# Kernel optimization log

Hardware: AMD Instinct MI355X
Metric: run time of the kernel (lower is better)

Reference implementation:

```python
import jax, jax.numpy as jnp
import numpy as np

B, N, D = 8, 2048, 1024
DC = 1024          # d_center
K = 4              # num_centers
NUM_JUMPS = 2
SPAN = 2
FIN = (2 + 2 * NUM_JUMPS + 1) * D  # 7*D

def _gelu(x):
    return jax.nn.gelu(x, approximate=False)  # torch nn.GELU default is exact erf

def setup_inputs() -> dict:
    key = jax.random.key(0)
    ks = jax.random.split(key, 16)
    s = lambda k, *sh: jax.random.normal(k, sh, dtype=jnp.float32) * 0.02
    return {
        "queries": jax.random.normal(ks[0], (B, N, D), dtype=jnp.float32),
        "fr_w1": s(ks[1], FIN, D), "fr_b1": jnp.zeros((D,), jnp.float32),
        "fr_w2": s(ks[2], D, D),   "fr_b2": jnp.zeros((D,), jnp.float32),
        "tc_w1": s(ks[3], D, DC),  "tc_b1": jnp.zeros((DC,), jnp.float32),
        "tc_w2": s(ks[4], DC, DC), "tc_b2": jnp.zeros((DC,), jnp.float32),
        "centers": jax.random.normal(ks[5], (K, DC), dtype=jnp.float32),
        "fc_w1": s(ks[6], D + DC, D), "fc_b1": jnp.zeros((D,), jnp.float32),
        "fc_w2": s(ks[7], D, D),      "fc_b2": jnp.zeros((D,), jnp.float32),
        "g_w": s(ks[8], D + DC, D),   "g_b": jnp.zeros((D,), jnp.float32),
    }

def reference(queries, fr_w1, fr_b1, fr_w2, fr_b2,
              tc_w1, tc_b1, tc_w2, tc_b2, centers,
              fc_w1, fc_b1, fc_w2, fc_b2, g_w, g_b):
    x = queries
    shifts = [1, -1, 0]  # left, right, x
    for i in range(1, NUM_JUMPS + 1):
        shifts += [i * SPAN, -i * SPAN]
    fusion = jnp.concatenate([jnp.roll(x, s, axis=1) for s in shifts], axis=-1)  # [B,N,7D]
    x_ring = _gelu(fusion @ fr_w1 + fr_b1) @ fr_w2 + fr_b2                       # [B,N,D]
    token_proj = _gelu(x_ring @ tc_w1 + tc_b1) @ tc_w2 + tc_b2                   # [B,N,DC]
    w = jax.nn.softmax(jnp.einsum('bnd,kd->bnk', token_proj, centers), axis=-1)  # [B,N,K]
    weighted = jnp.einsum('bnk,kd->bnd', w, centers)                             # [B,N,DC]
    fus2 = jnp.concatenate([x_ring, weighted], axis=-1)                          # [B,N,D+DC]
    gate = jax.nn.sigmoid(fus2 @ g_w + g_b)
    fc = _gelu(fus2 @ fc_w1 + fc_b1) @ fc_w2 + fc_b2
    return gate * fc + (1.0 - gate) * x_ring
```

## Files before the change

kernel.cpp:

```cpp
#include <hip/hip_runtime.h>
#include <hip/hip_bf16.h>
#include <math.h>

typedef unsigned short u16;
typedef __attribute__((ext_vector_type(8))) short short8;
typedef __attribute__((ext_vector_type(4))) float f32x4;


__device__ __forceinline__ float bf2f(u16 b) {
  return __uint_as_float(((unsigned int)b) << 16);
}
__device__ __forceinline__ u16 f2bf(float f) {
  unsigned int u = __float_as_uint(f);
  u += 0x7FFFu + ((u >> 16) & 1u);
  return (u16)(u >> 16);
}
__device__ __forceinline__ float gelu_exact(float x) {
  return 0.5f * x * (1.0f + erff(x * 0.70710678118654752f));
}

__device__ __forceinline__ void cp16(const void* g, void* l) {
  __builtin_amdgcn_global_load_lds(
      (const __attribute__((address_space(1))) unsigned int*)g,
      (__attribute__((address_space(3))) unsigned int*)l, 16, 0, 0);
}

template <int MODE, bool GATHER>
__global__ __launch_bounds__(512) void gemm256(
    const u16* __restrict__ A, int lda, const u16* __restrict__ Wt, int K,
    const float* __restrict__ bias, const float* __restrict__ bias2,
    void* __restrict__ out0, int ldo0, void* __restrict__ out1,
    void* __restrict__ out2, const float* __restrict__ p0,
    const float* __restrict__ p1, const float* __restrict__ p2) {
  extern __shared__ __align__(16) char sm[];
  const int tid = threadIdx.x;
  const int lane = tid & 63;
  const int wave = tid >> 6;
  const int wm = wave >> 2;
  const int wn = wave & 3;

  const unsigned linear = blockIdx.y * gridDim.x + blockIdx.x;
  const unsigned xcd = linear & 7u;
  const unsigned pos = linear >> 3;
  const unsigned bx = pos % gridDim.x;
  const unsigned by = xcd * (gridDim.y >> 3) + pos / gridDim.x;
  const int m0 = by * 256;
  const int n0 = bx * 256;

  const int sl = lane >> 3;
  const int qqs = (lane & 7) ^ sl;
  const int rowoff = sl * 2 + (qqs >> 2);
  const int colq = qqs & 3;

  const int r16 = lane & 15, q4 = lane >> 4;
  const int qqr = (((r16 & 1) << 2) | q4) ^ (r16 >> 1);
  const int laneA = wm * 8192 + (r16 >> 1) * 128 + qqr * 16;
  const int laneB = wn * 4096 + (r16 >> 1) * 128 + qqr * 16;

  const int nt = K >> 5;

  f32x4 acc[8][4];
#pragma unroll
  for (int i = 0; i < 8; i++)
#pragma unroll
    for (int j = 0; j < 4; j++) acc[i][j] = (f32x4){0.f, 0.f, 0.f, 0.f};

  auto a_src = [&](int t, int i) -> const u16* {
    const int chunk = wave + i * 8;
    const int row = chunk * 16 + rowoff;
    if (GATHER) {
      const int kg = t * 32 + colq * 8;
      const int seg = kg >> 10;
      int shift;
      switch (seg) {
        case 0: shift = 1; break;
        case 1: shift = -1; break;
        case 2: shift = 0; break;
        case 3: shift = 2; break;
        case 4: shift = -2; break;
        case 5: shift = 4; break;
        default: shift = -4; break;
      }
      const int m = m0 + row;
      const int b = m >> 11;
      const int nsrc = ((m & 2047) - shift) & 2047;
      return A + (long)((b << 11) | nsrc) * 1024 + (kg & 1023);
    }
    return A + (long)(m0 + row) * lda + t * 32 + colq * 8;
  };
  auto b_src = [&](int t, int i) -> const u16* {
    const int chunk = wave + i * 8;
    const int row = chunk * 16 + rowoff;
    return Wt + (long)(n0 + row) * K + t * 32 + colq * 8;
  };

  auto prefetch = [&](int s, short8 (&pbf)[4], short8 (&paf01)[2]) {
    const char* base = sm + ((s & 3) << 15);
#pragma unroll
    for (int ni = 0; ni < 4; ni++)
      pbf[ni] = *(const short8*)(base + 16384 + laneB + ni * 1024);
#pragma unroll
    for (int mi = 0; mi < 2; mi++)
      paf01[mi] = *(const short8*)(base + laneA + mi * 1024);
  };

  const u16 *pA0, *pA1, *pB0, *pB1;

  auto body = [&](int s, short8 (&cbf)[4], short8 (&caf01)[2],
                  short8 (&nbf)[4], short8 (&naf01)[2]) {
    const char* abase = sm + ((s & 3) << 15);
    short8 afr[6];
#pragma unroll
    for (int j = 0; j < 6; j++)
      afr[j] = *(const short8*)(abase + laneA + (j + 2) * 1024);
    prefetch(s + 1, nbf, naf01);

    const int sofs = ((s + 3) & 3) << 15;
    cp16(pA0, sm + sofs + wave * 1024);
    cp16(pA1, sm + sofs + (wave + 8) * 1024);
    cp16(pB0, sm + sofs + 16384 + wave * 1024);
    cp16(pB1, sm + sofs + 16384 + (wave + 8) * 1024);
    if (s + 4 <= nt - 1) {
      if (GATHER && (((s + 4) & 31) == 0)) {
        pA0 = a_src(s + 4, 0);
        pA1 = a_src(s + 4, 1);
      } else {
        pA0 += 32;
        pA1 += 32;
      }
      pB0 += 32;
      pB1 += 32;
    }

    asm volatile("s_waitcnt lgkmcnt(12)" ::: "memory");
    __builtin_amdgcn_sched_barrier(0);
    __builtin_amdgcn_s_setprio(1);
#pragma unroll
    for (int mi = 0; mi < 2; mi++)
#pragma unroll
      for (int ni = 0; ni < 4; ni++)
        acc[mi][ni] = __builtin_amdgcn_mfma_f32_16x16x32_bf16(
            caf01[mi], cbf[ni], acc[mi][ni], 0, 0, 0);

    asm volatile("s_waitcnt lgkmcnt(10)" ::: "memory");
    __builtin_amdgcn_sched_barrier(0);
#pragma unroll
    for (int j = 0; j < 2; j++)
#pragma unroll
      for (int ni = 0; ni < 4; ni++)
        acc[2 + j][ni] = __builtin_amdgcn_mfma_f32_16x16x32_bf16(
            afr[j], cbf[ni], acc[2 + j][ni], 0, 0, 0);

    asm volatile("s_waitcnt lgkmcnt(8)" ::: "memory");
    __builtin_amdgcn_sched_barrier(0);
#pragma unroll
    for (int j = 0; j < 2; j++)
#pragma unroll
      for (int ni = 0; ni < 4; ni++)
        acc[4 + j][ni] = __builtin_amdgcn_mfma_f32_16x16x32_bf16(
            afr[2 + j], cbf[ni], acc[4 + j][ni], 0, 0, 0);

    asm volatile("s_waitcnt lgkmcnt(6)" ::: "memory");
    __builtin_amdgcn_sched_barrier(0);
#pragma unroll
    for (int j = 0; j < 2; j++)
#pragma unroll
      for (int ni = 0; ni < 4; ni++)
        acc[6 + j][ni] = __builtin_amdgcn_mfma_f32_16x16x32_bf16(
            afr[4 + j], cbf[ni], acc[6 + j][ni], 0, 0, 0);
    __builtin_amdgcn_s_setprio(0);

    asm volatile("s_waitcnt vmcnt(4)" ::: "memory");
    __builtin_amdgcn_s_barrier();
  };

#pragma unroll
  for (int t = 0; t < 3; t++) {
    cp16(a_src(t, 0), sm + t * 32768 + wave * 1024);
    cp16(a_src(t, 1), sm + t * 32768 + (wave + 8) * 1024);
    cp16(b_src(t, 0), sm + t * 32768 + 16384 + wave * 1024);
    cp16(b_src(t, 1), sm + t * 32768 + 16384 + (wave + 8) * 1024);
  }
  pA0 = a_src(3, 0); pA1 = a_src(3, 1);
  pB0 = b_src(3, 0); pB1 = b_src(3, 1);
  asm volatile("s_waitcnt vmcnt(4)" ::: "memory");
  __builtin_amdgcn_s_barrier();

  short8 bfA[4], afA[2], bfB[4], afB[2];
  prefetch(0, bfA, afA);

  for (int s = 0; s < nt; s += 2) {
    body(s, bfA, afA, bfB, afB);
    body(s + 1, bfB, afB, bfA, afA);
  }
  asm volatile("s_waitcnt vmcnt(0) lgkmcnt(0)" ::: "memory");

  const int ccol = lane & 15;
  const int crow = (lane >> 4) * 4;
#pragma unroll
  for (int mi = 0; mi < 8; mi++) {
#pragma unroll
    for (int r = 0; r < 4; r++) {
      const int m = m0 + wm * 128 + mi * 16 + crow + r;
      float4 wrow;
      if (MODE == 8) wrow = *(const float4*)(p0 + (size_t)m * 4);
#pragma unroll
      for (int ni = 0; ni < 4; ni++) {
        const int n = n0 + wn * 64 + ni * 16 + ccol;
        const float v = acc[mi][ni][r];
        if (MODE == 0) {
          ((u16*)out0)[(long)m * ldo0 + n] = f2bf(gelu_exact(v + bias[n]));
        } else if (MODE == 4) {
          const float g = p0[(long)m * 1024 + n];
          const float xr = p1[(long)m * 1024 + n];
          ((float*)out0)[(long)m * ldo0 + n] =
              g * (v + bias[n]) + (1.0f - g) * xr;
        } else if (MODE == 6) {
          ((u16*)out0)[(long)m * ldo0 + n] = f2bf(v);
        } else if (MODE == 7) {
          if (n < 1024) {
            const float s = v + bias[n];
            ((float*)out1)[(long)m * 1024 + n] = s;
            ((u16*)out0)[(long)m * 1024 + n] = f2bf(s);
          } else {
            const int nn = n - 1024;
            ((u16*)out2)[(long)m * 1024 + nn] = f2bf(gelu_exact(v + bias2[nn]));
          }
        } else if (MODE == 8) {
          if (n < 1024) {
            const float4 g2 = *(const float4*)(p1 + (size_t)n * 4);
            const float s = v + bias[n] + wrow.x * g2.x + wrow.y * g2.y +
                            wrow.z * g2.z + wrow.w * g2.w;
            ((float*)out0)[(long)m * 1024 + n] = 1.0f / (1.0f + expf(-s));
          } else {
            const int nn = n - 1024;
            const float4 f2 = *(const float4*)(p2 + (size_t)nn * 4);
            const float s = v + bias2[nn] + wrow.x * f2.x + wrow.y * f2.y +
                            wrow.z * f2.z + wrow.w * f2.w;
            ((u16*)out1)[(long)m * 1024 + nn] = f2bf(gelu_exact(s));
          }
        }
      }
    }
  }
}

template <int MODE, bool GATHER>
__global__ __launch_bounds__(256) void gemm128(
    const u16* __restrict__ A, int lda, const u16* __restrict__ Wt, int K,
    const float* __restrict__ bias, const float* __restrict__ bias2,
    void* __restrict__ out0, int ldo0, void* __restrict__ out1,
    void* __restrict__ out2, const float* __restrict__ p0,
    const float* __restrict__ p1, const float* __restrict__ p2) {
  __shared__ __align__(16) u16 As[128 * 64];
  __shared__ __align__(16) u16 Bs[128 * 64];

  const int tid = threadIdx.x;
  const int lane = tid & 63;
  const int wave = tid >> 6;
  const int wm = wave >> 1;
  const int wn = wave & 1;

  const unsigned linear = blockIdx.y * gridDim.x + blockIdx.x;
  const unsigned xcd = linear & 7u;
  const unsigned pos = linear >> 3;
  const unsigned bx = pos % gridDim.x;
  const unsigned by = xcd * (gridDim.y >> 3) + pos / gridDim.x;
  const int m0 = by * 128;
  const int n0 = bx * 128;

  const int srow = lane >> 3;
  const int sq = lane & 7;
  const int sqs = sq ^ srow;

  f32x4 acc[4][4];
#pragma unroll
  for (int i = 0; i < 4; i++)
#pragma unroll
    for (int j = 0; j < 4; j++) acc[i][j] = (f32x4){0.f, 0.f, 0.f, 0.f};

  for (int k0 = 0; k0 < K; k0 += 64) {
#pragma unroll
    for (int i = 0; i < 4; i++) {
      const int rloc = wave * 32 + i * 8 + srow;
      const long gofs = (long)(m0 + rloc) * lda + k0 + sqs * 8;
      cp16(A + gofs, &As[(wave * 32 + i * 8) * 64]);
    }
#pragma unroll
    for (int i = 0; i < 4; i++) {
      const int rloc = wave * 32 + i * 8 + srow;
      const long gofs = (long)(n0 + rloc) * K + k0 + sqs * 8;
      cp16(Wt + gofs, &Bs[(wave * 32 + i * 8) * 64]);
    }
    __syncthreads();

    const int q4 = lane >> 4;
    const int r16 = lane & 15;
#pragma unroll
    for (int kk = 0; kk < 2; kk++) {
      short8 af[4], bf[4];
#pragma unroll
      for (int mi = 0; mi < 4; mi++) {
        const int row = wm * 64 + mi * 16 + r16;
        const int q = (kk * 4 + q4) ^ (row & 7);
        af[mi] = *(const short8*)&As[row * 64 + q * 8];
      }
#pragma unroll
      for (int ni = 0; ni < 4; ni++) {
        const int row = wn * 64 + ni * 16 + r16;
        const int q = (kk * 4 + q4) ^ (row & 7);
        bf[ni] = *(const short8*)&Bs[row * 64 + q * 8];
      }
#pragma unroll
      for (int mi = 0; mi < 4; mi++)
#pragma unroll
        for (int ni = 0; ni < 4; ni++)
          acc[mi][ni] = __builtin_amdgcn_mfma_f32_16x16x32_bf16(
              af[mi], bf[ni], acc[mi][ni], 0, 0, 0);
    }
    __syncthreads();
  }

  const int ccol = lane & 15;
  const int crow = (lane >> 4) * 4;
#pragma unroll
  for (int mi = 0; mi < 4; mi++) {
#pragma unroll
    for (int r = 0; r < 4; r++) {
      const int m = m0 + wm * 64 + mi * 16 + crow + r;
#pragma unroll
      for (int ni = 0; ni < 4; ni++) {
        const int n = n0 + wn * 64 + ni * 16 + ccol;
        const float v = acc[mi][ni][r];
        if (MODE == 6) {
          ((u16*)out0)[(long)m * ldo0 + n] = f2bf(v);
        }
      }
    }
  }
}

__global__ __launch_bounds__(256) void cast_bf16(const float* __restrict__ in,
                                                 u16* __restrict__ out, int n4) {
  const long i = (long)blockIdx.x * 256 + threadIdx.x;
  if (i < n4) {
    const float4 v = ((const float4*)in)[i];
    ushort4 o;
    o.x = f2bf(v.x); o.y = f2bf(v.y); o.z = f2bf(v.z); o.w = f2bf(v.w);
    ((ushort4*)out)[i] = o;
  }
}

__global__ __launch_bounds__(256) void transp_bf16(const float* __restrict__ in,
                                                   u16* __restrict__ out, int K,
                                                   int N) {
  __shared__ float tile[32][33];
  const int tx = threadIdx.x & 31;
  const int ty = threadIdx.x >> 5;
  const long r0 = (long)blockIdx.y * 32;
  const long c0 = (long)blockIdx.x * 32;
#pragma unroll
  for (int r = 0; r < 4; r++)
    tile[ty + r * 8][tx] = in[(r0 + ty + r * 8) * N + c0 + tx];
  __syncthreads();
#pragma unroll
  for (int r = 0; r < 4; r++)
    out[(c0 + ty + r * 8) * K + r0 + tx] = f2bf(tile[tx][ty + r * 8]);
}

__global__ __launch_bounds__(256) void transp7(
    const float* __restrict__ s0, const float* __restrict__ s1,
    const float* __restrict__ s2, const float* __restrict__ s3,
    const float* __restrict__ s4, const float* __restrict__ s5,
    const float* __restrict__ s6, u16* __restrict__ d0, u16* __restrict__ d1,
    u16* __restrict__ d2, u16* __restrict__ d3, u16* __restrict__ d4,
    u16* __restrict__ d5, u16* __restrict__ d6) {
  __shared__ float tile[32][33];
  const float* in;
  u16* out;
  switch (blockIdx.z) {
    case 0: in = s0; out = d0; break;
    case 1: in = s1; out = d1; break;
    case 2: in = s2; out = d2; break;
    case 3: in = s3; out = d3; break;
    case 4: in = s4; out = d4; break;
    case 5: in = s5; out = d5; break;
    default: in = s6; out = d6; break;
  }
  const int tx = threadIdx.x & 31;
  const int ty = threadIdx.x >> 5;
  const long r0 = (long)blockIdx.y * 32;
  const long c0 = (long)blockIdx.x * 32;
#pragma unroll
  for (int r = 0; r < 4; r++)
    tile[ty + r * 8][tx] = in[(r0 + ty + r * 8) * 1024 + c0 + tx];
  __syncthreads();
#pragma unroll
  for (int r = 0; r < 4; r++)
    out[(c0 + ty + r * 8) * 1024 + r0 + tx] = f2bf(tile[tx][ty + r * 8]);
}

__global__ __launch_bounds__(256) void fold_all(
    const u16* __restrict__ GbT, const u16* __restrict__ FbT,
    const u16* __restrict__ Wt3, const float* __restrict__ centers,
    const float* __restrict__ fr_b2, const float* __restrict__ tc_b1,
    const float* __restrict__ tc_w2, const float* __restrict__ tc_b2,
    float* __restrict__ G2T, float* __restrict__ F2T, float* __restrict__ c2,
    float* __restrict__ S, float* __restrict__ bc) {
  const int b = blockIdx.x;
  const int wave = threadIdx.x >> 6, lane = threadIdx.x & 63;
  if (b < 256) {
    const int n = b * 4 + wave;
    float g[4] = {0.f, 0.f, 0.f, 0.f}, f[4] = {0.f, 0.f, 0.f, 0.f};
#pragma unroll
    for (int p = 0; p < 2; p++) {
      const int base = p * 512 + lane * 8;
      const short8 gv = *(const short8*)(GbT + (long)n * 1024 + base);
      const short8 fv = *(const short8*)(FbT + (long)n * 1024 + base);
#pragma unroll
      for (int e = 0; e < 8; e++) {
        const float ge = bf2f((u16)gv[e]), fe = bf2f((u16)fv[e]);
#pragma unroll
        for (int k = 0; k < 4; k++) {
          const float c = centers[k * 1024 + base + e];
          g[k] += ge * c;
          f[k] += fe * c;
        }
      }
    }
#pragma unroll
    for (int k = 0; k < 4; k++)
#pragma unroll
      for (int off = 32; off > 0; off >>= 1) {
        g[k] += __shfl_xor(g[k], off);
        f[k] += __shfl_xor(f[k], off);
      }
    if (lane == 0) {
#pragma unroll
      for (int k = 0; k < 4; k++) {
        G2T[n * 4 + k] = g[k];
        F2T[n * 4 + k] = f[k];
      }
    }
  } else if (b < 512) {
    const int j = (b - 256) * 4 + wave;
    float s = 0.f;
#pragma unroll
    for (int p = 0; p < 2; p++) {
      const int base = p * 512 + lane * 8;
      const short8 wv = *(const short8*)(Wt3 + (long)j * 1024 + base);
#pragma unroll
      for (int e = 0; e < 8; e++) s += fr_b2[base + e] * bf2f((u16)wv[e]);
    }
#pragma unroll
    for (int off = 32; off > 0; off >>= 1) s += __shfl_xor(s, off);
    if (lane == 0) c2[j] = s + tc_b1[j];
  } else if (b < 768) {
    const int d = (b - 512) * 4 + wave;
    const float* row = tc_w2 + (long)d * 1024;
    float s0 = 0.f, s1 = 0.f, s2 = 0.f, s3 = 0.f;
    for (int e = lane; e < 1024; e += 64) {
      const float w = row[e];
      s0 += w * centers[e];
      s1 += w * centers[1024 + e];
      s2 += w * centers[2048 + e];
      s3 += w * centers[3072 + e];
    }
#pragma unroll
    for (int off = 32; off > 0; off >>= 1) {
      s0 += __shfl_xor(s0, off);
      s1 += __shfl_xor(s1, off);
      s2 += __shfl_xor(s2, off);
      s3 += __shfl_xor(s3, off);
    }
    if (lane == 0) {
      S[d] = s0; S[1024 + d] = s1; S[2048 + d] = s2; S[3072 + d] = s3;
    }
  } else {
    const int k = wave;
    float s = 0.f;
    for (int e = lane; e < 1024; e += 64) s += tc_b2[e] * centers[k * 1024 + e];
#pragma unroll
    for (int off = 32; off > 0; off >>= 1) s += __shfl_xor(s, off);
    if (lane == 0) bc[k] = s;
  }
}

__global__ __launch_bounds__(256) void centers_kernel(
    const u16* __restrict__ h2, const float* __restrict__ S,
    const float* __restrict__ bc, float* __restrict__ wtok) {
  const int lane = threadIdx.x & 63;
  const int wave = threadIdx.x >> 6;
  const long t = (long)blockIdx.x * 4 + wave;
  const u16* row = h2 + t * 1024;
  float d0 = 0.f, d1 = 0.f, d2 = 0.f, d3 = 0.f;
#pragma unroll
  for (int j = 0; j < 2; j++) {
    const int dbase = j * 512 + lane * 8;
    const short8 v = *(const short8*)(row + dbase);
#pragma unroll
    for (int e = 0; e < 8; e++) {
      const float x = bf2f((u16)v[e]);
      const int d = dbase + e;
      d0 += x * S[d];
      d1 += x * S[1024 + d];
      d2 += x * S[2048 + d];
      d3 += x * S[3072 + d];
    }
  }
#pragma unroll
  for (int off = 32; off > 0; off >>= 1) {
    d0 += __shfl_xor(d0, off);
    d1 += __shfl_xor(d1, off);
    d2 += __shfl_xor(d2, off);
    d3 += __shfl_xor(d3, off);
  }
  if (lane == 0) {
    d0 += bc[0]; d1 += bc[1]; d2 += bc[2]; d3 += bc[3];
    const float mx = fmaxf(fmaxf(d0, d1), fmaxf(d2, d3));
    float e0 = expf(d0 - mx), e1 = expf(d1 - mx), e2 = expf(d2 - mx),
          e3 = expf(d3 - mx);
    const float inv = 1.0f / (e0 + e1 + e2 + e3);
    *(float4*)(wtok + t * 4) = (float4){e0 * inv, e1 * inv, e2 * inv, e3 * inv};
  }
}

extern "C" void kernel_launch(void* const* d_in, const int* in_sizes, int n_in,
                              void* d_out, int out_size, void* d_ws,
                              size_t ws_size, hipStream_t stream) {
  const float* queries = (const float*)d_in[0];
  const float* fr_w1 = (const float*)d_in[1];
  const float* fr_b1 = (const float*)d_in[2];
  const float* fr_w2 = (const float*)d_in[3];
  const float* fr_b2 = (const float*)d_in[4];
  const float* tc_w1 = (const float*)d_in[5];
  const float* tc_b1 = (const float*)d_in[6];
  const float* tc_w2 = (const float*)d_in[7];
  const float* tc_b2 = (const float*)d_in[8];
  const float* centers = (const float*)d_in[9];
  const float* fc_w1 = (const float*)d_in[10];
  const float* fc_b1 = (const float*)d_in[11];
  const float* fc_w2 = (const float*)d_in[12];
  const float* fc_b2 = (const float*)d_in[13];
  const float* g_w = (const float*)d_in[14];
  const float* g_b = (const float*)d_in[15];

  char* ws = (char*)d_ws;
  u16* Wt1 = (u16*)ws; ws += (size_t)7168 * 1024 * 2;
  u16* Wt3 = (u16*)ws; ws += (size_t)1024 * 1024 * 2;
  u16* Wt6 = (u16*)ws; ws += (size_t)1024 * 1024 * 2;
  u16* WtJ = (u16*)ws; ws += (size_t)2048 * 1024 * 2;
  u16* WtG2 = (u16*)ws; ws += (size_t)2048 * 1024 * 2;
  u16* Fw2b = (u16*)ws; ws += (size_t)1024 * 1024 * 2;
  u16* GbT = (u16*)ws; ws += (size_t)1024 * 1024 * 2;
  u16* FbT = (u16*)ws; ws += (size_t)1024 * 1024 * 2;
  u16* Xb = (u16*)ws;  ws += (size_t)16384 * 1024 * 2;
  u16* h1 = (u16*)ws;  ws += (size_t)16384 * 1024 * 2;
  u16* xrb = (u16*)ws; ws += (size_t)16384 * 1024 * 2;
  float* xring = (float*)ws; ws += (size_t)16384 * 1024 * 4;
  float* wtok = (float*)ws; ws += (size_t)16384 * 4 * 4;
  float* S = (float*)ws; ws += (size_t)4 * 1024 * 4;
  float* G2T = (float*)ws; ws += (size_t)1024 * 4 * 4;
  float* F2T = (float*)ws; ws += (size_t)1024 * 4 * 4;
  float* c2 = (float*)ws; ws += (size_t)1024 * 4;
  float* bc = (float*)ws; ws += 16;
  float* gate = (float*)d_out;
  float* out = (float*)d_out;

  static bool attr_set = false;
  if (!attr_set) {
    attr_set = true;
    (void)hipFuncSetAttribute((const void*)gemm256<0, true>,
                              hipFuncAttributeMaxDynamicSharedMemorySize,
                              131072);
    (void)hipFuncSetAttribute((const void*)gemm256<7, false>,
                              hipFuncAttributeMaxDynamicSharedMemorySize,
                              131072);
    (void)hipFuncSetAttribute((const void*)gemm256<8, false>,
                              hipFuncAttributeMaxDynamicSharedMemorySize,
                              131072);
    (void)hipFuncSetAttribute((const void*)gemm256<4, false>,
                              hipFuncAttributeMaxDynamicSharedMemorySize,
                              131072);
  }

  cast_bf16<<<16384, 256, 0, stream>>>(queries, Xb, 16384 * 1024 / 4);
  cast_bf16<<<1024, 256, 0, stream>>>(fr_w2, Fw2b, 1024 * 1024 / 4);
  transp_bf16<<<dim3(32, 224), 256, 0, stream>>>(fr_w1, Wt1, 7168, 1024);
  transp7<<<dim3(32, 32, 7), 256, 0, stream>>>(
      tc_w1, fc_w2, fr_w2, g_w, fc_w1, g_w + (size_t)1024 * 1024,
      fc_w1 + (size_t)1024 * 1024, Wt3, Wt6, WtJ, WtG2,
      WtG2 + (size_t)1024 * 1024, GbT, FbT);
  fold_all<<<769, 256, 0, stream>>>(GbT, FbT, Wt3, centers, fr_b2, tc_b1,
                                    tc_w2, tc_b2, G2T, F2T, c2, S, bc);
  gemm128<6, false><<<dim3(8, 8), 256, 0, stream>>>(
      Wt3, 1024, Fw2b, 1024, nullptr, nullptr, WtJ + (size_t)1024 * 1024, 1024,
      nullptr, nullptr, nullptr, nullptr, nullptr);

  gemm256<0, true><<<dim3(4, 64), 512, 131072, stream>>>(
      Xb, 0, Wt1, 7168, fr_b1, nullptr, h1, 1024, nullptr, nullptr, nullptr,
      nullptr, nullptr);
  gemm256<7, false><<<dim3(8, 64), 512, 131072, stream>>>(
      h1, 1024, WtJ, 1024, fr_b2, c2, xrb, 1024, xring, Xb, nullptr, nullptr,
      nullptr);
  centers_kernel<<<4096, 256, 0, stream>>>(Xb, S, bc, wtok);
  gemm256<8, false><<<dim3(8, 64), 512, 131072, stream>>>(
      xrb, 1024, WtG2, 1024, g_b, fc_b1, gate, 1024, h1, nullptr, wtok, G2T,
      F2T);
  gemm256<4, false><<<dim3(4, 64), 512, 131072, stream>>>(
      h1, 1024, Wt6, 1024, fc_b2, nullptr, out, 1024, nullptr, nullptr, gate,
      xring, nullptr);
}
```

Measured before the change: 770.0 us.

## Switch 256x256 GEMM to 4 waves with 128x128 per-wave tiles

Rebuilds the main bf16 GEMM to run 256 threads (4 waves in a 2x2 grid) instead of 512, so each wave computes a 128x128 output tile (8x8 MFMA fragments) instead of 128x64. This halves B-fragment LDS reads per MFMA and doubles per-thread global-to-LDS copies. The MFMA groups are reordered so the first group issues before the prefetch and copy instructions, with the wait counts adjusted to match. The cost is far higher accumulator register pressure (256 floats per thread) and fewer waves to hide latency, which risks spills or stalls.

Measured after the change: 1.208 ms. 56.9% more time.

```diff
diff --git a/kernel.cpp b/kernel.cpp
--- a/kernel.cpp
+++ b/kernel.cpp
@@ -26,7 +26,7 @@
 }
 
 template <int MODE, bool GATHER>
-__global__ __launch_bounds__(512) void gemm256(
+__global__ __launch_bounds__(256, 1) void gemm256(
     const u16* __restrict__ A, int lda, const u16* __restrict__ Wt, int K,
     const float* __restrict__ bias, const float* __restrict__ bias2,
     void* __restrict__ out0, int ldo0, void* __restrict__ out1,
@@ -36,8 +36,8 @@
   const int tid = threadIdx.x;
   const int lane = tid & 63;
   const int wave = tid >> 6;
-  const int wm = wave >> 2;
-  const int wn = wave & 3;
+  const int wm = wave >> 1;
+  const int wn = wave & 1;
 
   const unsigned linear = blockIdx.y * gridDim.x + blockIdx.x;
   const unsigned xcd = linear & 7u;
@@ -54,19 +54,20 @@
 
   const int r16 = lane & 15, q4 = lane >> 4;
   const int qqr = (((r16 & 1) << 2) | q4) ^ (r16 >> 1);
-  const int laneA = wm * 8192 + (r16 >> 1) * 128 + qqr * 16;
-  const int laneB = wn * 4096 + (r16 >> 1) * 128 + qqr * 16;
+  const int laneRC = (r16 >> 1) * 128 + qqr * 16;
+  const int laneA = wm * 8192 + laneRC;
+  const int laneB = 16384 + wn * 8192 + laneRC;
 
   const int nt = K >> 5;
 
-  f32x4 acc[8][4];
+  f32x4 acc[8][8];
 #pragma unroll
   for (int i = 0; i < 8; i++)
 #pragma unroll
-    for (int j = 0; j < 4; j++) acc[i][j] = (f32x4){0.f, 0.f, 0.f, 0.f};
+    for (int j = 0; j < 8; j++) acc[i][j] = (f32x4){0.f, 0.f, 0.f, 0.f};
 
   auto a_src = [&](int t, int i) -> const u16* {
-    const int chunk = wave + i * 8;
+    const int chunk = wave + i * 4;
     const int row = chunk * 16 + rowoff;
     if (GATHER) {
       const int kg = t * 32 + colq * 8;
@@ -89,104 +90,116 @@
     return A + (long)(m0 + row) * lda + t * 32 + colq * 8;
   };
   auto b_src = [&](int t, int i) -> const u16* {
-    const int chunk = wave + i * 8;
+    const int chunk = wave + i * 4;
     const int row = chunk * 16 + rowoff;
     return Wt + (long)(n0 + row) * K + t * 32 + colq * 8;
   };
 
-  auto prefetch = [&](int s, short8 (&pbf)[4], short8 (&paf01)[2]) {
+  auto prefetch = [&](int s, short8 (&pbf)[8], short8 (&paf)[2]) {
     const char* base = sm + ((s & 3) << 15);
 #pragma unroll
-    for (int ni = 0; ni < 4; ni++)
-      pbf[ni] = *(const short8*)(base + 16384 + laneB + ni * 1024);
+    for (int ni = 0; ni < 8; ni++)
+      pbf[ni] = *(const short8*)(base + laneB + ni * 1024);
 #pragma unroll
     for (int mi = 0; mi < 2; mi++)
-      paf01[mi] = *(const short8*)(base + laneA + mi * 1024);
+      paf[mi] = *(const short8*)(base + laneA + mi * 1024);
   };
 
-  const u16 *pA0, *pA1, *pB0, *pB1;
-
-  auto body = [&](int s, short8 (&cbf)[4], short8 (&caf01)[2],
-                  short8 (&nbf)[4], short8 (&naf01)[2]) {
+  const u16 *pA0, *pA1, *pA2, *pA3, *pB0, *pB1, *pB2, *pB3;
+
+  auto body = [&](int s, short8 (&cbf)[8], short8 (&caf)[2],
+                  short8 (&nbf)[8], short8 (&naf)[2]) {
     const char* abase = sm + ((s & 3) << 15);
     short8 afr[6];
 #pragma unroll
     for (int j = 0; j < 6; j++)
       afr[j] = *(const short8*)(abase + laneA + (j + 2) * 1024);
-    prefetch(s + 1, nbf, naf01);
-
+
+    asm volatile("s_waitcnt lgkmcnt(6)" ::: "memory");
+    __builtin_amdgcn_sched_barrier(0);
+    __builtin_amdgcn_s_setprio(1);
+#pragma unroll
+    for (int mi = 0; mi < 2; mi++)
+#pragma unroll
+      for (int ni = 0; ni < 8; ni++)
+        acc[mi][ni] = __builtin_amdgcn_mfma_f32_16x16x32_bf16(
+            caf[mi], cbf[ni], acc[mi][ni], 0, 0, 0);
+    __builtin_amdgcn_s_setprio(0);
+    __builtin_amdgcn_sched_barrier(0);
+
+    prefetch(s + 1, nbf, naf);
     const int sofs = ((s + 3) & 3) << 15;
-    cp16(pA0, sm + sofs + wave * 1024);
-    cp16(pA1, sm + sofs + (wave + 8) * 1024);
-    cp16(pB0, sm + sofs + 16384 + wave * 1024);
-    cp16(pB1, sm + sofs + 16384 + (wave + 8) * 1024);
+    cp16(pA0, sm + sofs + (wave + 0) * 1024);
+    cp16(pA1, sm + sofs + (wave + 4) * 1024);
+    cp16(pA2, sm + sofs + (wave + 8) * 1024);
+    cp16(pA3, sm + sofs + (wave + 12) * 1024);
+    cp16(pB0, sm + sofs + 16384 + (wave + 0) * 1024);
+    cp16(pB1, sm + sofs + 16384 + (wave + 4) * 1024);
+    cp16(pB2, sm + sofs + 16384 + (wave + 8) * 1024);
+    cp16(pB3, sm + sofs + 16384 + (wave + 12) * 1024);
     if (s + 4 <= nt - 1) {
       if (GATHER && (((s + 4) & 31) == 0)) {
         pA0 = a_src(s + 4, 0);
         pA1 = a_src(s + 4, 1);
+        pA2 = a_src(s + 4, 2);
+        pA3 = a_src(s + 4, 3);
       } else {
-        pA0 += 32;
-        pA1 += 32;
-      }
-      pB0 += 32;
-      pB1 += 32;
-    }
+        pA0 += 32; pA1 += 32; pA2 += 32; pA3 += 32;
+      }
+      pB0 += 32; pB1 += 32; pB2 += 32; pB3 += 32;
+    }
+
+    asm volatile("s_waitcnt lgkmcnt(14)" ::: "memory");
+    __builtin_amdgcn_sched_barrier(0);
+    __builtin_amdgcn_s_setprio(1);
+#pragma unroll
+    for (int j = 0; j < 2; j++)
+#pragma unroll
+      for (int ni = 0; ni < 8; ni++)
+        acc[2 + j][ni] = __builtin_amdgcn_mfma_f32_16x16x32_bf16(
+            afr[j], cbf[ni], acc[2 + j][ni], 0, 0, 0);
+    __builtin_amdgcn_s_setprio(0);
 
     asm volatile("s_waitcnt lgkmcnt(12)" ::: "memory");
     __builtin_amdgcn_sched_barrier(0);
     __builtin_amdgcn_s_setprio(1);
 #pragma unroll
-    for (int mi = 0; mi < 2; mi++)
-#pragma unroll
-      for (int ni = 0; ni < 4; ni++)
-        acc[mi][ni] = __builtin_amdgcn_mfma_f32_16x16x32_bf16(
-            caf01[mi], cbf[ni], acc[mi][ni], 0, 0, 0);
+    for (int j = 0; j < 2; j++)
+#pragma unroll
+      for (int ni = 0; ni < 8; ni++)
+        acc[4 + j][ni] = __builtin_amdgcn_mfma_f32_16x16x32_bf16(
+            afr[2 + j], cbf[ni], acc[4 + j][ni], 0, 0, 0);
+    __builtin_amdgcn_s_setprio(0);
 
     asm volatile("s_waitcnt lgkmcnt(10)" ::: "memory");
     __builtin_amdgcn_sched_barrier(0);
+    __builtin_amdgcn_s_setprio(1);
 #pragma unroll
     for (int j = 0; j < 2; j++)
 #pragma unroll
-      for (int ni = 0; ni < 4; ni++)
-        acc[2 + j][ni] = __builtin_amdgcn_mfma_f32_16x16x32_bf16(
-            afr[j], cbf[ni], acc[2 + j][ni], 0, 0, 0);
-
-    asm volatile("s_waitcnt lgkmcnt(8)" ::: "memory");
-    __builtin_amdgcn_sched_barrier(0);
-#pragma unroll
-    for (int j = 0; j < 2; j++)
-#pragma unroll
-      for (int ni = 0; ni < 4; ni++)
-        acc[4 + j][ni] = __builtin_amdgcn_mfma_f32_16x16x32_bf16(
-            afr[2 + j], cbf[ni], acc[4 + j][ni], 0, 0, 0);
-
-    asm volatile("s_waitcnt lgkmcnt(6)" ::: "memory");
-    __builtin_amdgcn_sched_barrier(0);
-#pragma unroll
-    for (int j = 0; j < 2; j++)
-#pragma unroll
-      for (int ni = 0; ni < 4; ni++)
+      for (int ni = 0; ni < 8; ni++)
         acc[6 + j][ni] = __builtin_amdgcn_mfma_f32_16x16x32_bf16(
             afr[4 + j], cbf[ni], acc[6 + j][ni], 0, 0, 0);
     __builtin_amdgcn_s_setprio(0);
 
-    asm volatile("s_waitcnt vmcnt(4)" ::: "memory");
+    asm volatile("s_waitcnt vmcnt(8)" ::: "memory");
     __builtin_amdgcn_s_barrier();
   };
 
 #pragma unroll
   for (int t = 0; t < 3; t++) {
-    cp16(a_src(t, 0), sm + t * 32768 + wave * 1024);
-    cp16(a_src(t, 1), sm + t * 32768 + (wave + 8) * 1024);
-    cp16(b_src(t, 0), sm + t * 32768 + 16384 + wave * 1024);
-    cp16(b_src(t, 1), sm + t * 32768 + 16384 + (wave + 8) * 1024);
-  }
-  pA0 = a_src(3, 0); pA1 = a_src(3, 1);
-  pB0 = b_src(3, 0); pB1 = b_src(3, 1);
-  asm volatile("s_waitcnt vmcnt(4)" ::: "memory");
+#pragma unroll
+    for (int i = 0; i < 4; i++) {
+      cp16(a_src(t, i), sm + t * 32768 + (wave + i * 4) * 1024);
+      cp16(b_src(t, i), sm + t * 32768 + 16384 + (wave + i * 4) * 1024);
+    }
+  }
+  pA0 = a_src(3, 0); pA1 = a_src(3, 1); pA2 = a_src(3, 2); pA3 = a_src(3, 3);
+  pB0 = b_src(3, 0); pB1 = b_src(3, 1); pB2 = b_src(3, 2); pB3 = b_src(3, 3);
+  asm volatile("s_waitcnt vmcnt(8)" ::: "memory");
   __builtin_amdgcn_s_barrier();
 
-  short8 bfA[4], afA[2], bfB[4], afB[2];
+  short8 bfA[8], afA[2], bfB[8], afB[2];
   prefetch(0, bfA, afA);
 
   for (int s = 0; s < nt; s += 2) {
@@ -205,8 +218,8 @@
       float4 wrow;
       if (MODE == 8) wrow = *(const float4*)(p0 + (size_t)m * 4);
 #pragma unroll
-      for (int ni = 0; ni < 4; ni++) {
-        const int n = n0 + wn * 64 + ni * 16 + ccol;
+      for (int ni = 0; ni < 8; ni++) {
+        const int n = n0 + wn * 128 + ni * 16 + ccol;
         const float v = acc[mi][ni][r];
         if (MODE == 0) {
           ((u16*)out0)[(long)m * ldo0 + n] = f2bf(gelu_exact(v + bias[n]));
@@ -597,17 +610,17 @@
       Wt3, 1024, Fw2b, 1024, nullptr, nullptr, WtJ + (size_t)1024 * 1024, 1024,
       nullptr, nullptr, nullptr, nullptr, nullptr);
 
-  gemm256<0, true><<<dim3(4, 64), 512, 131072, stream>>>(
+  gemm256<0, true><<<dim3(4, 64), 256, 131072, stream>>>(
       Xb, 0, Wt1, 7168, fr_b1, nullptr, h1, 1024, nullptr, nullptr, nullptr,
       nullptr, nullptr);
-  gemm256<7, false><<<dim3(8, 64), 512, 131072, stream>>>(
+  gemm256<7, false><<<dim3(8, 64), 256, 131072, stream>>>(
       h1, 1024, WtJ, 1024, fr_b2, c2, xrb, 1024, xring, Xb, nullptr, nullptr,
       nullptr);
   centers_kernel<<<4096, 256, 0, stream>>>(Xb, S, bc, wtok);
-  gemm256<8, false><<<dim3(8, 64), 512, 131072, stream>>>(
+  gemm256<8, false><<<dim3(8, 64), 256, 131072, stream>>>(
       xrb, 1024, WtG2, 1024, g_b, fc_b1, gate, 1024, h1, nullptr, wtok, G2T,
       F2T);
-  gemm256<4, false><<<dim3(4, 64), 512, 131072, stream>>>(
+  gemm256<4, false><<<dim3(4, 64), 256, 131072, stream>>>(
       h1, 1024, Wt6, 1024, fc_b2, nullptr, out, 1024, nullptr, nullptr, gate,
       xring, nullptr);
 }
```
